# Kernel tuning notes

Measured on AMD Instinct MI355X. Metric: run time of the kernel, lower is better.

The kernel has to match this reference:

```python
import jax, jax.numpy as jnp
import numpy as np

DIM = 256
NUM_HEADS = 8
HEAD_DIM = 64
NUM_MEM_KV = 4
HIDDEN = NUM_HEADS * HEAD_DIM  # 512


def rmsnorm(x, g):
    # F.normalize(x, dim=1) * g * sqrt(C)
    c = x.shape[1]
    n = jnp.sqrt(jnp.sum(x * x, axis=1, keepdims=True))
    xn = x / jnp.maximum(n, 1e-12)
    return xn * g * (c ** 0.5)


def setup_inputs() -> dict:
    key = jax.random.key(0)
    ks = jax.random.split(key, 7)
    b, h, w = 16, 64, 64
    x = jax.random.normal(ks[0], (b, DIM, h, w), dtype=jnp.float32)
    g_in = jnp.ones((1, DIM, 1, 1), dtype=jnp.float32)
    w_qkv = jax.random.normal(ks[1], (HIDDEN * 3, DIM), dtype=jnp.float32) * (1.0 / np.sqrt(DIM))
    mem_kv = jax.random.normal(ks[2], (2, NUM_HEADS, HEAD_DIM, NUM_MEM_KV), dtype=jnp.float32)
    w_out = jax.random.normal(ks[3], (DIM, HIDDEN), dtype=jnp.float32) * (1.0 / np.sqrt(HIDDEN))
    b_out = jax.random.normal(ks[4], (DIM,), dtype=jnp.float32) * 0.01
    g_out = jnp.ones((1, DIM, 1, 1), dtype=jnp.float32)
    return {"x": x, "g_in": g_in, "w_qkv": w_qkv, "mem_kv": mem_kv,
            "w_out": w_out, "b_out": b_out, "g_out": g_out}


def reference(x, g_in, w_qkv, mem_kv, w_out, b_out, g_out):
    b, c, h, w = x.shape
    scale = HEAD_DIM ** (-0.5)
    xn = rmsnorm(x, g_in)
    # 1x1 conv (no bias) as GEMM: [b, 3*hidden, h, w]
    qkv = jnp.einsum('bcxy,oc->boxy', xn, w_qkv)
    q, k, v = jnp.split(qkv, 3, axis=1)
    # b (heads d) x y -> b heads d n
    def to_heads(t):
        return t.reshape(b, NUM_HEADS, HEAD_DIM, h * w)
    q, k, v = to_heads(q), to_heads(k), to_heads(v)
    mem_k = jnp.broadcast_to(mem_kv[0], (b, NUM_HEADS, HEAD_DIM, NUM_MEM_KV))
    mem_v = jnp.broadcast_to(mem_kv[1], (b, NUM_HEADS, HEAD_DIM, NUM_MEM_KV))
    k = jnp.concatenate([mem_k, k], axis=-1)
    v = jnp.concatenate([mem_v, v], axis=-1)
    q = jax.nn.softmax(q, axis=-2) * scale   # softmax over head_dim
    k = jax.nn.softmax(k, axis=-1)           # softmax over sequence
    context = jnp.einsum('bhdn,bhen->bhde', k, v)  # [b,h,d,d] per-head context
    out = jnp.einsum('bhde,bhdn->bhen', context, q)  # [b,h,d,n]
    out = out.reshape(b, HIDDEN, h, w)
    out = jnp.einsum('bcxy,oc->boxy', out, w_out) + b_out[None, :, None, None]
    return rmsnorm(out, g_out)
```

## Files before the change

kernel.cpp:

```cpp
#include <hip/hip_runtime.h>
#include <hip/hip_bf16.h>

typedef __hip_bfloat16 bf16;
typedef short bf16x8 __attribute__((ext_vector_type(8)));
typedef float f32x4 __attribute__((ext_vector_type(4)));

#define PTOT  65536
#define NPOS  4096
#define CIN   256
#define HID   512
#define HD    64

__device__ __forceinline__ float us2f(unsigned short u) {
    return __uint_as_float(((unsigned int)u) << 16);
}
__device__ __forceinline__ float ldf(const void* p, size_t i, bool bf) {
    return bf ? us2f(((const unsigned short*)p)[i]) : ((const float*)p)[i];
}
__device__ __forceinline__ unsigned short f2bs(float v) {
    __hip_bfloat16 h = __float2bfloat16(v);
    return *reinterpret_cast<unsigned short*>(&h);
}
__device__ __forceinline__ void gld16(const void* g, void* s) {
    __builtin_amdgcn_global_load_lds(
        (const __attribute__((address_space(1))) unsigned int*)g,
        (__attribute__((address_space(3))) unsigned int*)s, 16, 0, 0);
}

__global__ __launch_bounds__(256) void k_detect(const unsigned* __restrict__ x,
                                                int* __restrict__ flag) {
    int t = threadIdx.x;
    unsigned w = x[(size_t)t * 997];
    unsigned e7 = (w >> 8) & 0x7f;
    __shared__ int s[256];
    s[t] = (e7 >= 58 && e7 <= 66) ? 1 : 0;
    __syncthreads();
    for (int k = 128; k > 0; k >>= 1) { if (t < k) s[t] += s[t + k]; __syncthreads(); }
    if (t == 0) flag[0] = (s[0] >= 128) ? 1 : 0;
}

__global__ void k_relay(const int* __restrict__ src, int* __restrict__ dst) {
    dst[0] = src[0];
}

__global__ __launch_bounds__(256) void k_cvt(const void* __restrict__ src,
        unsigned short* __restrict__ dst, int n, const int* __restrict__ flag) {
    bool bf = flag[0] != 0;
    int i = blockIdx.x * 256 + threadIdx.x;
    if (i < n) dst[i] = f2bs(ldf(src, i, bf));
}

template<bool BF>
__device__ __forceinline__ void norm_xn_body(const void* __restrict__ x,
        const void* __restrict__ g, unsigned short* __restrict__ xn,
        float* __restrict__ smem)
{
    float* xs   = smem;
    float* gS   = smem + 17216;
    float* red2 = smem + 17472;
    float* sS   = smem + 18496;
    const int t = threadIdx.x;
    const int p0 = blockIdx.x * 64;
    const int b = p0 >> 12;
    const int posbase = p0 & 4095;
    gS[t] = ldf(g, t, BF);
    __syncthreads();
    const int pl4 = (t & 15) * 4;
    const int crow = t >> 4;
    const size_t xbase = ((size_t)b * CIN) << 12;
    float ssq[4] = {0.f, 0.f, 0.f, 0.f};
    #pragma unroll
    for (int rr = 0; rr < 16; ++rr) {
        int c = rr * 16 + crow;
        float v[4];
        if (BF) {
            ushort4 u = *(const ushort4*)((const unsigned short*)x + xbase +
                                          ((size_t)c << 12) + posbase + pl4);
            v[0] = us2f(u.x); v[1] = us2f(u.y); v[2] = us2f(u.z); v[3] = us2f(u.w);
        } else {
            float4 f = *(const float4*)((const float*)x + xbase +
                                        ((size_t)c << 12) + posbase + pl4);
            v[0] = f.x; v[1] = f.y; v[2] = f.z; v[3] = f.w;
        }
        float gv = gS[c];
        float* row = xs + (c >> 6) * 4304 + (c & 63) * 67;
        #pragma unroll
        for (int e = 0; e < 4; ++e) {
            ssq[e] += v[e] * v[e];
            row[pl4 + e] = v[e] * gv;
        }
    }
    #pragma unroll
    for (int e = 0; e < 4; ++e) red2[crow * 64 + pl4 + e] = ssq[e];
    __syncthreads();
    if (t < 64) {
        float tot = 0.f;
        #pragma unroll
        for (int j = 0; j < 16; ++j) tot += red2[j * 64 + t];
        sS[t] = 16.0f / fmaxf(sqrtf(tot), 1e-12f);
    }
    __syncthreads();
    const int pr = t >> 2, c0 = (t & 3) * 64;
    const float sc = sS[pr];
    const float* base = xs + (t & 3) * 4304 + pr;
    unsigned short* dst = &xn[(size_t)(p0 + pr) * 256 + c0];
    #pragma unroll
    for (int q = 0; q < 4; ++q) {
        unsigned short tmp[16];
        #pragma unroll
        for (int j = 0; j < 16; ++j)
            tmp[j] = f2bs(base[(q * 16 + j) * 67] * sc);
        *(uint4*)(dst + q * 16)     = ((uint4*)tmp)[0];
        *(uint4*)(dst + q * 16 + 8) = ((uint4*)tmp)[1];
    }
}
__global__ __launch_bounds__(256) void k_norm_xn(
        const void* __restrict__ x, const void* __restrict__ g,
        unsigned short* __restrict__ xn, const int* __restrict__ flag)
{
    __shared__ float smem[18560];
    if (flag[0]) norm_xn_body<true>(x, g, xn, smem);
    else         norm_xn_body<false>(x, g, xn, smem);
}

template<int KTOT, bool BIAS, int OSTRIDE>
__global__ __launch_bounds__(256) void k_mfma(
        const bf16* __restrict__ Am, const bf16* __restrict__ Bm,
        const void* __restrict__ bias, bf16* __restrict__ C,
        const int* __restrict__ flag)
{
    __shared__ __align__(16) unsigned short As[128 * 32];
    __shared__ __align__(16) unsigned short Bs[128 * 32];
    const int tid = threadIdx.x;
    const int wv = tid >> 6, lane = tid & 63;
    const int quad = lane >> 4, l16 = lane & 15;
    const int wm = wv >> 1, wn = wv & 1;
    const int m0 = blockIdx.y * 128, n0 = blockIdx.x * 128;
    f32x4 acc[4][4] = {};
    const bf16* gA = Am + (size_t)(m0 + (tid >> 2)) * KTOT + (tid & 3) * 8;
    const bf16* gB = Bm + (size_t)(n0 + (tid >> 2)) * KTOT + (tid & 3) * 8;
    unsigned short* lA = As + wv * 512;
    unsigned short* lB = Bs + wv * 512;
    for (int k0 = 0; k0 < KTOT; k0 += 32) {
        gld16(gA + k0, lA);
        gld16(gA + (size_t)64 * KTOT + k0, lA + 2048);
        gld16(gB + k0, lB);
        gld16(gB + (size_t)64 * KTOT + k0, lB + 2048);
        __syncthreads();
        bf16x8 bfr[4];
        #pragma unroll
        for (int j = 0; j < 4; ++j)
            bfr[j] = *(const bf16x8*)&Bs[(wn * 64 + j * 16 + l16) * 32 + quad * 8];
        #pragma unroll
        for (int i = 0; i < 4; ++i) {
            bf16x8 af = *(const bf16x8*)&As[(wm * 64 + i * 16 + l16) * 32 + quad * 8];
            #pragma unroll
            for (int j = 0; j < 4; ++j)
                acc[i][j] = __builtin_amdgcn_mfma_f32_16x16x32_bf16(af, bfr[j], acc[i][j], 0, 0, 0);
        }
        __syncthreads();
    }
    bool bf = BIAS ? (flag[0] != 0) : false;
    #pragma unroll
    for (int i = 0; i < 4; ++i) {
        int row = m0 + wm * 64 + i * 16 + quad * 4;
        #pragma unroll
        for (int r = 0; r < 4; ++r) {
            float bv = BIAS ? ldf(bias, row + r, bf) : 0.0f;
            #pragma unroll
            for (int j = 0; j < 4; ++j) {
                int col = n0 + wn * 64 + j * 16 + l16;
                C[(size_t)(row + r) * OSTRIDE + col] = __float2bfloat16(acc[i][j][r] + bv);
            }
        }
    }
}

__global__ __launch_bounds__(512) void k_kvgemm(
        const bf16* __restrict__ Am, const bf16* __restrict__ Bm,
        bf16* __restrict__ C)
{
    __shared__ __align__(16) unsigned short As[128 * 256];
    __shared__ __align__(16) unsigned short Bs[2][64 * 256];
    const int t = threadIdx.x;
    const int w = t >> 6, lane = t & 63;
    const int quad = lane >> 4, l16 = lane & 15;
    const int wm = w >> 1, wn = w & 1;
    const int p = blockIdx.x;
    const int xcd = p & 7, slot = p >> 3;
    const int chunk = xcd * 4 + (slot & 3);
    const int mt = slot >> 2;
    const int m0 = mt * 128;
    const size_t cbase = (size_t)chunk * 2048;

    const int srow = t >> 5;
    const int sks  = (t & 31) ^ (srow & 7);

    #pragma unroll
    for (int q = 0; q < 8; ++q)
        gld16(Am + (size_t)(m0 + q * 16 + srow) * 256 + sks * 8,
              (char*)As + q * 8192 + w * 1024);
    #pragma unroll
    for (int q = 0; q < 4; ++q)
        gld16(Bm + (cbase + q * 16 + srow) * 256 + sks * 8,
              (char*)Bs[0] + q * 8192 + w * 1024);
    #pragma unroll
    for (int q = 0; q < 4; ++q)
        gld16(Bm + (cbase + 64 + q * 16 + srow) * 256 + sks * 8,
              (char*)Bs[1] + q * 8192 + w * 1024);

    asm volatile("s_waitcnt vmcnt(8)" ::: "memory");
    __builtin_amdgcn_s_barrier();
    asm volatile("" ::: "memory");

    bf16x8 af[2][8];
    #pragma unroll
    for (int i = 0; i < 2; ++i) {
        int row = wm * 32 + i * 16 + l16;
        #pragma unroll
        for (int kk = 0; kk < 8; ++kk)
            af[i][kk] = *(const bf16x8*)((const char*)As + row * 512 +
                         (((kk * 4 + quad) ^ (row & 7)) << 4));
    }

    for (int s = 0; s < 32; ++s) {
        if (s > 0) {
            asm volatile("" ::: "memory");
            __builtin_amdgcn_s_barrier();
            asm volatile("" ::: "memory");
            if (s + 1 < 32) {
                #pragma unroll
                for (int q = 0; q < 4; ++q)
                    gld16(Bm + (cbase + (size_t)(s + 1) * 64 + q * 16 + srow) * 256 + sks * 8,
                          (char*)Bs[(s + 1) & 1] + q * 8192 + w * 1024);
            }
        }
        if (s == 0)      asm volatile("s_waitcnt vmcnt(4)"  ::: "memory");
        else if (s < 31) asm volatile("s_waitcnt vmcnt(20)" ::: "memory");
        else             asm volatile("s_waitcnt vmcnt(16)" ::: "memory");
        __builtin_amdgcn_s_barrier();
        asm volatile("" ::: "memory");

        const unsigned short* Bbuf = Bs[s & 1];
        f32x4 acc[2][2] = {};
        #pragma unroll
        for (int kk = 0; kk < 8; ++kk) {
            bf16x8 bfr[2];
            #pragma unroll
            for (int j = 0; j < 2; ++j) {
                int row = wn * 32 + j * 16 + l16;
                bfr[j] = *(const bf16x8*)((const char*)Bbuf + row * 512 +
                          (((kk * 4 + quad) ^ (row & 7)) << 4));
            }
            #pragma unroll
            for (int i = 0; i < 2; ++i)
                #pragma unroll
                for (int j = 0; j < 2; ++j)
                    acc[i][j] = __builtin_amdgcn_mfma_f32_16x16x32_bf16(af[i][kk], bfr[j], acc[i][j], 0, 0, 0);
        }
        #pragma unroll
        for (int i = 0; i < 2; ++i) {
            #pragma unroll
            for (int r = 0; r < 4; ++r) {
                int row = m0 + wm * 32 + i * 16 + quad * 4 + r;
                size_t col = cbase + (size_t)s * 64 + wn * 32;
                #pragma unroll
                for (int j = 0; j < 2; ++j)
                    C[(size_t)row * PTOT + col + j * 16 + l16] = __float2bfloat16(acc[i][j][r]);
            }
        }
    }
}

__global__ __launch_bounds__(256) void k_qapply(
        const bf16* __restrict__ xn, const bf16* __restrict__ wq,
        const unsigned short* __restrict__ ct_bf,
        unsigned short* __restrict__ oat_pe)
{
    __shared__ __align__(16) unsigned short smem[128 * 136 + 2 * 64 * 72];
    unsigned short* As  = smem;
    unsigned short* Bs  = smem + 8192;
    unsigned short* As2 = smem;
    unsigned short* ctS = smem + 17408;
    const int tid = threadIdx.x;
    const int wv = tid >> 6, lane = tid & 63;
    const int quad = lane >> 4, l16 = lane & 15;
    const int wm = wv >> 1, wn = wv & 1;
    const int n0 = blockIdx.x * 128;
    const int m0 = blockIdx.y * 128;
    const int b = m0 >> 12;

    {
        int hh = tid >> 7, tt = tid & 127;
        int bh = (b << 3) + (n0 >> 6) + hh;
        int e = tt >> 1, d0 = (tt & 1) * 32;
        const unsigned short* src = ct_bf + (size_t)bh * 4096 + e * 64 + d0;
        unsigned short* dst = ctS + hh * 4608 + e * 72 + d0;
        *(uint4*)dst        = *(const uint4*)src;
        *(uint4*)(dst + 8)  = *(const uint4*)(src + 8);
        *(uint4*)(dst + 16) = *(const uint4*)(src + 16);
        *(uint4*)(dst + 24) = *(const uint4*)(src + 24);
    }

    f32x4 acc[4][4] = {};
    const bf16* gA = xn + (size_t)(m0 + (tid >> 2)) * CIN + (tid & 3) * 8;
    const bf16* gB = wq + (size_t)(n0 + (tid >> 2)) * CIN + (tid & 3) * 8;
    unsigned short* lA = As + wv * 512;
    unsigned short* lB = Bs + wv * 512;
    for (int k0 = 0; k0 < CIN; k0 += 32) {
        gld16(gA + k0, lA);
        gld16(gA + (size_t)64 * CIN + k0, lA + 2048);
        gld16(gB + k0, lB);
        gld16(gB + (size_t)64 * CIN + k0, lB + 2048);
        __syncthreads();
        bf16x8 bfr[4];
        #pragma unroll
        for (int j = 0; j < 4; ++j)
            bfr[j] = *(const bf16x8*)&Bs[(wn * 64 + j * 16 + l16) * 32 + quad * 8];
        #pragma unroll
        for (int i = 0; i < 4; ++i) {
            bf16x8 af = *(const bf16x8*)&As[(wm * 64 + i * 16 + l16) * 32 + quad * 8];
            #pragma unroll
            for (int j = 0; j < 4; ++j)
                acc[i][j] = __builtin_amdgcn_mfma_f32_16x16x32_bf16(af, bfr[j], acc[i][j], 0, 0, 0);
        }
        __syncthreads();
    }

    #pragma unroll
    for (int i = 0; i < 4; ++i) {
        #pragma unroll
        for (int r = 0; r < 4; ++r) {
            float m = fmaxf(fmaxf(acc[i][0][r], acc[i][1][r]),
                            fmaxf(acc[i][2][r], acc[i][3][r]));
            #pragma unroll
            for (int s = 1; s < 16; s <<= 1)
                m = fmaxf(m, __shfl_xor(m, s));
            float ev[4];
            float sum = 0.f;
            #pragma unroll
            for (int j = 0; j < 4; ++j) { ev[j] = expf(acc[i][j][r] - m); sum += ev[j]; }
            #pragma unroll
            for (int s = 1; s < 16; s <<= 1)
                sum += __shfl_xor(sum, s);
            float inv = 0.125f / sum;
            int row = wm * 64 + i * 16 + quad * 4 + r;
            #pragma unroll
            for (int j = 0; j < 4; ++j)
                As2[row * 136 + wn * 64 + j * 16 + l16] = f2bs(ev[j] * inv);
        }
    }
    __syncthreads();

    f32x4 acc2[4][4] = {};
    #pragma unroll
    for (int kk = 0; kk < 2; ++kk) {
        bf16x8 bfr[4];
        #pragma unroll
        for (int j = 0; j < 4; ++j)
            bfr[j] = *(const bf16x8*)&ctS[wn * 4608 + (j * 16 + l16) * 72 + kk * 32 + quad * 8];
        #pragma unroll
        for (int i = 0; i < 4; ++i) {
            bf16x8 af = *(const bf16x8*)&As2[(wm * 64 + i * 16 + l16) * 136 + wn * 64 + kk * 32 + quad * 8];
            #pragma unroll
            for (int j = 0; j < 4; ++j)
                acc2[i][j] = __builtin_amdgcn_mfma_f32_16x16x32_bf16(af, bfr[j], acc2[i][j], 0, 0, 0);
        }
    }
    #pragma unroll
    for (int i = 0; i < 4; ++i) {
        #pragma unroll
        for (int r = 0; r < 4; ++r) {
            int prow = wm * 64 + i * 16 + quad * 4 + r;
            unsigned short* obase = oat_pe + (size_t)(m0 + prow) * HID + n0 + wn * 64;
            #pragma unroll
            for (int j = 0; j < 4; ++j)
                obase[j * 16 + l16] = f2bs(acc2[i][j][r]);
        }
    }
}

__global__ __launch_bounds__(256) void k_kstats(
        const bf16* __restrict__ kv, const void* __restrict__ memkv,
        float* __restrict__ rowmax, float* __restrict__ rowinv,
        const int* __restrict__ flag)
{
    bool bf = flag[0] != 0;
    int r = blockIdx.x;
    int b = r >> 9, hd = r & 511;
    const unsigned short* krow = (const unsigned short*)kv + (size_t)hd * PTOT + b * NPOS;
    int t = threadIdx.x;
    float vals[16];
    float m = -1e30f;
    #pragma unroll
    for (int i = 0; i < 16; ++i) {
        vals[i] = us2f(krow[t + (i << 8)]);
        m = fmaxf(m, vals[i]);
    }
    float mv = (t < 4) ? ldf(memkv, hd * 4 + t, bf) : -1e30f;
    m = fmaxf(m, mv);
    __shared__ float red[256];
    red[t] = m; __syncthreads();
    for (int s = 128; s > 0; s >>= 1) {
        if (t < s) red[t] = fmaxf(red[t], red[t + s]);
        __syncthreads();
    }
    float M = red[0]; __syncthreads();
    float sum = 0.f;
    #pragma unroll
    for (int i = 0; i < 16; ++i) sum += expf(vals[i] - M);
    if (t < 4) sum += expf(mv - M);
    red[t] = sum; __syncthreads();
    for (int s = 128; s > 0; s >>= 1) {
        if (t < s) red[t] += red[t + s];
        __syncthreads();
    }
    if (t == 0) { rowmax[r] = M; rowinv[r] = 1.0f / red[0]; }
}

__global__ __launch_bounds__(256) void k_context_mfma(
        const bf16* __restrict__ kv, const void* __restrict__ memkv,
        const float* __restrict__ rowmax, const float* __restrict__ rowinv,
        float* __restrict__ ctpart, const int* __restrict__ flag)
{
    bool bf = flag[0] != 0;
    int bh = blockIdx.x, chunk = blockIdx.y;
    int b = bh >> 3, h = bh & 7;
    __shared__ __align__(16) unsigned short As[4][64 * 32];
    __shared__ __align__(16) unsigned short Bs[4][64 * 32];
    __shared__ float rmS[64], riS[64];
    const int tid = threadIdx.x;
    if (tid < 64) {
        rmS[tid] = rowmax[(b << 9) + (h << 6) + tid];
        riS[tid] = rowinv[(b << 9) + (h << 6) + tid];
    }
    __syncthreads();
    const int wv = tid >> 6, lane = tid & 63;
    const int quad = lane >> 4, l16 = lane & 15;
    const int wm = wv >> 1, wn = wv & 1;
    const int krow = tid >> 2, kseg = tid & 3;
    const float rm = rmS[krow], ri = riS[krow];
    const unsigned short* kbase = (const unsigned short*)kv + (size_t)(h * HD) * PTOT + b * NPOS + chunk * 1024;
    const unsigned short* vbase = (const unsigned short*)kv + (size_t)(HID + h * HD) * PTOT + b * NPOS + chunk * 1024;
    f32x4 acc[2][2] = {};
    for (int s = 0; s < 8; ++s) {
        int nb = s * 128;
        #pragma unroll
        for (int kk = 0; kk < 4; ++kk) {
            uint4 u = *(const uint4*)(kbase + (size_t)krow * PTOT + nb + kk * 32 + kseg * 8);
            unsigned short out[8];
            const unsigned short* us = (const unsigned short*)&u;
            #pragma unroll
            for (int e = 0; e < 8; ++e)
                out[e] = f2bs(expf(us2f(us[e]) - rm) * ri);
            *(uint4*)&As[kk][krow * 32 + kseg * 8] = *(uint4*)out;
        }
        #pragma unroll
        for (int kk = 0; kk < 4; ++kk)
            gld16(vbase + (size_t)(wv * 16 + (lane >> 2)) * PTOT + nb + kk * 32 + (lane & 3) * 8,
                  &Bs[kk][wv * 512]);
        __syncthreads();
        #pragma unroll
        for (int kk = 0; kk < 4; ++kk) {
            bf16x8 bfr[2];
            #pragma unroll
            for (int j = 0; j < 2; ++j)
                bfr[j] = *(const bf16x8*)&Bs[kk][(wn * 32 + j * 16 + l16) * 32 + quad * 8];
            #pragma unroll
            for (int i = 0; i < 2; ++i) {
                bf16x8 af = *(const bf16x8*)&As[kk][(wm * 32 + i * 16 + l16) * 32 + quad * 8];
                #pragma unroll
                for (int j = 0; j < 2; ++j)
                    acc[i][j] = __builtin_amdgcn_mfma_f32_16x16x32_bf16(af, bfr[j], acc[i][j], 0, 0, 0);
            }
        }
        __syncthreads();
    }
    if (chunk == 0) {
        float mv[2][4];
        #pragma unroll
        for (int j = 0; j < 2; ++j) {
            int e = wn * 32 + j * 16 + l16;
            #pragma unroll
            for (int mm = 0; mm < 4; ++mm)
                mv[j][mm] = ldf(memkv, 2048 + ((h << 6) + e) * 4 + mm, bf);
        }
        #pragma unroll
        for (int i = 0; i < 2; ++i) {
            #pragma unroll
            for (int r = 0; r < 4; ++r) {
                int d = wm * 32 + i * 16 + quad * 4 + r;
                #pragma unroll
                for (int mm = 0; mm < 4; ++mm) {
                    float kw = expf(ldf(memkv, ((h << 6) + d) * 4 + mm, bf) - rmS[d]) * riS[d];
                    #pragma unroll
                    for (int j = 0; j < 2; ++j)
                        acc[i][j][r] = fmaf(kw, mv[j][mm], acc[i][j][r]);
                }
            }
        }
    }
    float* outp = ctpart + (size_t)(chunk * 128 + bh) * 4096;
    #pragma unroll
    for (int i = 0; i < 2; ++i) {
        #pragma unroll
        for (int r = 0; r < 4; ++r) {
            int d = wm * 32 + i * 16 + quad * 4 + r;
            #pragma unroll
            for (int j = 0; j < 2; ++j) {
                int e = wn * 32 + j * 16 + l16;
                outp[d * 64 + e] = acc[i][j][r];
            }
        }
    }
}

__global__ __launch_bounds__(256) void k_ctsum(
        const float* __restrict__ ctpart, unsigned short* __restrict__ ct_bf)
{
    int bh = blockIdx.x, t = threadIdx.x;
    int i0 = t * 16;
    int e = i0 >> 6, d0 = i0 & 63;
    unsigned short tmp[16];
    #pragma unroll
    for (int j = 0; j < 16; ++j) {
        int d = d0 + j;
        float s = 0.f;
        #pragma unroll
        for (int c = 0; c < 4; ++c)
            s += ctpart[(size_t)(c * 128 + bh) * 4096 + d * 64 + e];
        tmp[j] = f2bs(s);
    }
    unsigned short* dst = ct_bf + (size_t)bh * 4096 + i0;
    *(uint4*)dst = ((uint4*)tmp)[0];
    *(uint4*)(dst + 8) = ((uint4*)tmp)[1];
}

template<bool BF>
__device__ __forceinline__ void rmsout_body(const unsigned short* __restrict__ pre,
        const void* __restrict__ g, void* __restrict__ out, float* __restrict__ smem)
{
    float* gS   = smem;
    float* red2 = smem + 256;
    float* sS   = smem + 1280;
    const int t = threadIdx.x;
    const int p0 = blockIdx.x * 64;
    const int b = p0 >> 12;
    const int posbase = p0 & 4095;
    gS[t] = ldf(g, t, BF);
    const int pl4 = (t & 15) * 4;
    const int crow = t >> 4;
    const unsigned short* pbase = pre + p0 + pl4;
    ushort4 u[16];
    float ssq[4] = {0.f, 0.f, 0.f, 0.f};
    #pragma unroll
    for (int rr = 0; rr < 16; ++rr) {
        int c = rr * 16 + crow;
        u[rr] = *(const ushort4*)(pbase + (size_t)c * PTOT);
        float v0 = us2f(u[rr].x), v1 = us2f(u[rr].y), v2 = us2f(u[rr].z), v3 = us2f(u[rr].w);
        ssq[0] += v0 * v0; ssq[1] += v1 * v1; ssq[2] += v2 * v2; ssq[3] += v3 * v3;
    }
    #pragma unroll
    for (int e = 0; e < 4; ++e) red2[crow * 64 + pl4 + e] = ssq[e];
    __syncthreads();
    if (t < 64) {
        float tot = 0.f;
        #pragma unroll
        for (int j = 0; j < 16; ++j) tot += red2[j * 64 + t];
        sS[t] = 16.0f / fmaxf(sqrtf(tot), 1e-12f);
    }
    __syncthreads();
    const float s0 = sS[pl4], s1 = sS[pl4 + 1], s2 = sS[pl4 + 2], s3 = sS[pl4 + 3];
    #pragma unroll
    for (int rr = 0; rr < 16; ++rr) {
        int c = rr * 16 + crow;
        float gv = gS[c];
        float v0 = us2f(u[rr].x) * s0 * gv;
        float v1 = us2f(u[rr].y) * s1 * gv;
        float v2 = us2f(u[rr].z) * s2 * gv;
        float v3 = us2f(u[rr].w) * s3 * gv;
        size_t oi = ((size_t)(b * CIN + c) << 12) + posbase + pl4;
        if (BF) {
            ushort4 o;
            o.x = f2bs(v0); o.y = f2bs(v1); o.z = f2bs(v2); o.w = f2bs(v3);
            *(ushort4*)((unsigned short*)out + oi) = o;
        } else {
            float4 o; o.x = v0; o.y = v1; o.z = v2; o.w = v3;
            *(float4*)((float*)out + oi) = o;
        }
    }
}
__global__ __launch_bounds__(256) void k_rmsnorm_out(
        const unsigned short* __restrict__ pre, const void* __restrict__ g,
        void* __restrict__ out, const int* __restrict__ flag)
{
    __shared__ float smem[1344];
    if (flag[0]) rmsout_body<true>(pre, g, out, smem);
    else         rmsout_body<false>(pre, g, out, smem);
}

extern "C" void kernel_launch(void* const* d_in, const int* in_sizes, int n_in,
                              void* d_out, int out_size, void* d_ws, size_t ws_size,
                              hipStream_t stream) {
    const void* x     = d_in[0];
    const void* g_in  = d_in[1];
    const void* w_qkv = d_in[2];
    const void* memkv = d_in[3];
    const void* w_out = d_in[4];
    const void* b_out = d_in[5];
    const void* g_out = d_in[6];

    char* ws = (char*)d_ws;
    bf16*           kv     = (bf16*)ws;
    unsigned short* oat_pe = (unsigned short*)(ws + 67108864);
    unsigned short* pre    = (unsigned short*)ws;
    int*            flagB  = (int*)(ws + 50331648);

    char* ob = (char*)d_out;
    float*          ctpart = (float*)ob;
    float*          rowmax = (float*)(ob + 8388608);
    float*          rowinv = (float*)(ob + 8421376);
    int*            flagA  = (int*)(ob + 8454144);
    unsigned short* wq_b   = (unsigned short*)(ob + 9437184);
    unsigned short* wout_b = (unsigned short*)(ob + 10485760);
    unsigned short* ct_bf  = (unsigned short*)(ob + 11010048);
    unsigned short* xn     = (unsigned short*)(ob + 12582912);

    k_detect<<<1, 256, 0, stream>>>((const unsigned*)x, flagA);

    k_cvt<<<1536, 256, 0, stream>>>(w_qkv, wq_b, 1536 * 256, flagA);
    k_cvt<<<512, 256, 0, stream>>>(w_out, wout_b, 256 * 512, flagA);

    k_norm_xn<<<1024, 256, 0, stream>>>(x, g_in, xn, flagA);

    k_kvgemm<<<256, 512, 0, stream>>>(
        (const bf16*)(wq_b + (size_t)512 * CIN), (const bf16*)xn, kv);

    k_kstats<<<8192, 256, 0, stream>>>(kv, memkv, rowmax, rowinv, flagA);

    dim3 gctx(128, 4);
    k_context_mfma<<<gctx, 256, 0, stream>>>(kv, memkv, rowmax, rowinv, ctpart, flagA);

    k_ctsum<<<128, 256, 0, stream>>>(ctpart, ct_bf);

    dim3 gqa(4, 512);
    k_qapply<<<gqa, 256, 0, stream>>>(
        (const bf16*)xn, (const bf16*)wq_b, ct_bf, oat_pe);

    dim3 go(512, 2);
    k_mfma<HID, true, PTOT><<<go, 256, 0, stream>>>(
        (const bf16*)wout_b, (const bf16*)oat_pe, b_out, (bf16*)pre, flagA);

    k_relay<<<1, 1, 0, stream>>>(flagA, flagB);

    k_rmsnorm_out<<<1024, 256, 0, stream>>>(pre, g_out, d_out, flagB);
}
```

Measured before the change: 351.3 us.

## Restructure q-apply kernel as persistent weight-resident loop with double-buffered xn tiles

The q-projection, softmax and context-apply kernel now launches 256 blocks of 512 threads. Each block keeps its 128-channel weight slice and two heads' context matrices resident in 144KB of LDS, loaded once through XOR-swizzled direct-to-LDS loads. It then streams 16 tiles of 64 positions, double-buffering the xn loads with explicit vmcnt waits. The softmax goes through an fp32 staging buffer in LDS. This avoids reloading weights and context for every 128-position tile, at the cost of much lower occupancy, extra barriers per tile and smaller MFMA tiles per wave.

```diff
diff --git a/kernel.cpp b/kernel.cpp
--- a/kernel.cpp
+++ b/kernel.cpp
@@ -272,110 +272,174 @@
     }
 }
 
-__global__ __launch_bounds__(256) void k_qapply(
+__global__ __launch_bounds__(512) void k_qapply(
         const bf16* __restrict__ xn, const bf16* __restrict__ wq,
         const unsigned short* __restrict__ ct_bf,
         unsigned short* __restrict__ oat_pe)
 {
-    __shared__ __align__(16) unsigned short smem[128 * 136 + 2 * 64 * 72];
-    unsigned short* As  = smem;
-    unsigned short* Bs  = smem + 8192;
-    unsigned short* As2 = smem;
-    unsigned short* ctS = smem + 17408;
-    const int tid = threadIdx.x;
-    const int wv = tid >> 6, lane = tid & 63;
+    __shared__ __align__(16) char smem[147456];
+    unsigned short* As  = (unsigned short*)smem;
+    unsigned short* Bs  = (unsigned short*)(smem + 65536);
+    unsigned short* ctS = (unsigned short*)(smem + 131072);
+    float*          S32 = (float*)smem;
+    unsigned short* qsm = (unsigned short*)(smem + 33792);
+    const int t = threadIdx.x;
+    const int w = t >> 6, lane = t & 63;
     const int quad = lane >> 4, l16 = lane & 15;
-    const int wm = wv >> 1, wn = wv & 1;
-    const int n0 = blockIdx.x * 128;
-    const int m0 = blockIdx.y * 128;
-    const int b = m0 >> 12;
-
-    {
-        int hh = tid >> 7, tt = tid & 127;
-        int bh = (b << 3) + (n0 >> 6) + hh;
-        int e = tt >> 1, d0 = (tt & 1) * 32;
-        const unsigned short* src = ct_bf + (size_t)bh * 4096 + e * 64 + d0;
-        unsigned short* dst = ctS + hh * 4608 + e * 72 + d0;
-        *(uint4*)dst        = *(const uint4*)src;
-        *(uint4*)(dst + 8)  = *(const uint4*)(src + 8);
-        *(uint4*)(dst + 16) = *(const uint4*)(src + 16);
-        *(uint4*)(dst + 24) = *(const uint4*)(src + 24);
-    }
-
-    f32x4 acc[4][4] = {};
-    const bf16* gA = xn + (size_t)(m0 + (tid >> 2)) * CIN + (tid & 3) * 8;
-    const bf16* gB = wq + (size_t)(n0 + (tid >> 2)) * CIN + (tid & 3) * 8;
-    unsigned short* lA = As + wv * 512;
-    unsigned short* lB = Bs + wv * 512;
-    for (int k0 = 0; k0 < CIN; k0 += 32) {
-        gld16(gA + k0, lA);
-        gld16(gA + (size_t)64 * CIN + k0, lA + 2048);
-        gld16(gB + k0, lB);
-        gld16(gB + (size_t)64 * CIN + k0, lB + 2048);
-        __syncthreads();
-        bf16x8 bfr[4];
-        #pragma unroll
-        for (int j = 0; j < 4; ++j)
-            bfr[j] = *(const bf16x8*)&Bs[(wn * 64 + j * 16 + l16) * 32 + quad * 8];
-        #pragma unroll
-        for (int i = 0; i < 4; ++i) {
-            bf16x8 af = *(const bf16x8*)&As[(wm * 64 + i * 16 + l16) * 32 + quad * 8];
-            #pragma unroll
-            for (int j = 0; j < 4; ++j)
-                acc[i][j] = __builtin_amdgcn_mfma_f32_16x16x32_bf16(af, bfr[j], acc[i][j], 0, 0, 0);
-        }
-        __syncthreads();
-    }
-
-    #pragma unroll
-    for (int i = 0; i < 4; ++i) {
-        #pragma unroll
-        for (int r = 0; r < 4; ++r) {
-            float m = fmaxf(fmaxf(acc[i][0][r], acc[i][1][r]),
-                            fmaxf(acc[i][2][r], acc[i][3][r]));
-            #pragma unroll
-            for (int s = 1; s < 16; s <<= 1)
-                m = fmaxf(m, __shfl_xor(m, s));
-            float ev[4];
-            float sum = 0.f;
-            #pragma unroll
-            for (int j = 0; j < 4; ++j) { ev[j] = expf(acc[i][j][r] - m); sum += ev[j]; }
-            #pragma unroll
-            for (int s = 1; s < 16; s <<= 1)
-                sum += __shfl_xor(sum, s);
+    const int wm = w >> 1, wn = w & 1;
+    const int ct4 = blockIdx.x & 3;
+    const int chunk = blockIdx.x >> 2;
+    const int n0 = ct4 * 128;
+    const size_t P0 = (size_t)chunk * 1024;
+    const int b = (int)(P0 >> 12);
+    const int srow = t >> 5, sks = (t & 31) ^ (srow & 7);
+
+    #pragma unroll
+    for (int q = 0; q < 8; ++q)
+        gld16(wq + (size_t)(n0 + q * 16 + srow) * 256 + sks * 8,
+              smem + q * 8192 + w * 1024);
+    #pragma unroll
+    for (int k = 0; k < 2; ++k) {
+        int u = k * 512 + t;
+        int hh = u >> 9, e = (u >> 3) & 63, slot = u & 7;
+        gld16(ct_bf + (size_t)(b * 8 + ct4 * 2 + hh) * 4096 + e * 64 + ((slot ^ (e & 7)) * 8),
+              (char*)ctS + k * 8192 + w * 1024);
+    }
+    #pragma unroll
+    for (int q = 0; q < 4; ++q)
+        gld16(xn + (P0 + q * 16 + srow) * 256 + sks * 8,
+              (char*)Bs + q * 8192 + w * 1024);
+    #pragma unroll
+    for (int q = 0; q < 4; ++q)
+        gld16(xn + (P0 + 64 + q * 16 + srow) * 256 + sks * 8,
+              (char*)Bs + 32768 + q * 8192 + w * 1024);
+
+    asm volatile("s_waitcnt vmcnt(10)" ::: "memory");
+    __builtin_amdgcn_s_barrier();
+    asm volatile("" ::: "memory");
+
+    bf16x8 af[2][8];
+    #pragma unroll
+    for (int i = 0; i < 2; ++i) {
+        int row = wm * 32 + i * 16 + l16;
+        #pragma unroll
+        for (int kk = 0; kk < 8; ++kk)
+            af[i][kk] = *(const bf16x8*)((const char*)As + row * 512 +
+                         (((kk * 4 + quad) ^ (row & 7)) << 4));
+    }
+
+    const int smrow = t >> 2, smseg = t & 3;
+    const int smpos = smrow >> 1, smhead = smrow & 1;
+    const int hh = w >> 2, pm = (w >> 1) & 1, pn = w & 1;
+
+    for (int s = 0; s < 16; ++s) {
+        if (s > 0 && s + 1 < 16) {
+            #pragma unroll
+            for (int q = 0; q < 4; ++q)
+                gld16(xn + (P0 + (size_t)(s + 1) * 64 + q * 16 + srow) * 256 + sks * 8,
+                      (char*)Bs + ((s + 1) & 1) * 32768 + q * 8192 + w * 1024);
+        }
+        if (s == 0)      asm volatile("s_waitcnt vmcnt(4)"  ::: "memory");
+        else if (s < 15) asm volatile("s_waitcnt vmcnt(20)" ::: "memory");
+        else             asm volatile("s_waitcnt vmcnt(16)" ::: "memory");
+        __builtin_amdgcn_s_barrier();
+        asm volatile("" ::: "memory");
+
+        const char* Bbuf = (const char*)Bs + (s & 1) * 32768;
+        f32x4 acc[2][2] = {};
+        #pragma unroll
+        for (int kk = 0; kk < 8; ++kk) {
+            bf16x8 bfr[2];
+            #pragma unroll
+            for (int j = 0; j < 2; ++j) {
+                int row = wn * 32 + j * 16 + l16;
+                bfr[j] = *(const bf16x8*)(Bbuf + row * 512 +
+                          (((kk * 4 + quad) ^ (row & 7)) << 4));
+            }
+            #pragma unroll
+            for (int i = 0; i < 2; ++i)
+                #pragma unroll
+                for (int j = 0; j < 2; ++j)
+                    acc[i][j] = __builtin_amdgcn_mfma_f32_16x16x32_bf16(af[i][kk], bfr[j], acc[i][j], 0, 0, 0);
+        }
+        #pragma unroll
+        for (int i = 0; i < 2; ++i)
+            #pragma unroll
+            for (int j = 0; j < 2; ++j) {
+                int pos = wn * 32 + j * 16 + l16;
+                int chb = wm * 32 + i * 16 + quad * 4;
+                #pragma unroll
+                for (int r = 0; r < 4; ++r)
+                    S32[pos * 132 + chb + r] = acc[i][j][r];
+            }
+        asm volatile("s_waitcnt lgkmcnt(0)" ::: "memory");
+        __builtin_amdgcn_s_barrier();
+        asm volatile("" ::: "memory");
+
+        {
+            const float* srp = S32 + smpos * 132 + smhead * 64 + smseg * 16;
+            f32x4 v[4];
+            #pragma unroll
+            for (int q = 0; q < 4; ++q) v[q] = *(const f32x4*)(srp + q * 4);
+            float m = v[0][0];
+            #pragma unroll
+            for (int q = 0; q < 4; ++q)
+                #pragma unroll
+                for (int e = 0; e < 4; ++e) m = fmaxf(m, v[q][e]);
+            m = fmaxf(m, __shfl_xor(m, 1));
+            m = fmaxf(m, __shfl_xor(m, 2));
+            float ev[16], sum = 0.f;
+            #pragma unroll
+            for (int q = 0; q < 4; ++q)
+                #pragma unroll
+                for (int e = 0; e < 4; ++e) {
+                    float x = expf(v[q][e] - m);
+                    ev[q * 4 + e] = x; sum += x;
+                }
+            sum += __shfl_xor(sum, 1);
+            sum += __shfl_xor(sum, 2);
             float inv = 0.125f / sum;
-            int row = wm * 64 + i * 16 + quad * 4 + r;
-            #pragma unroll
-            for (int j = 0; j < 4; ++j)
-                As2[row * 136 + wn * 64 + j * 16 + l16] = f2bs(ev[j] * inv);
-        }
-    }
-    __syncthreads();
-
-    f32x4 acc2[4][4] = {};
-    #pragma unroll
-    for (int kk = 0; kk < 2; ++kk) {
-        bf16x8 bfr[4];
-        #pragma unroll
-        for (int j = 0; j < 4; ++j)
-            bfr[j] = *(const bf16x8*)&ctS[wn * 4608 + (j * 16 + l16) * 72 + kk * 32 + quad * 8];
-        #pragma unroll
-        for (int i = 0; i < 4; ++i) {
-            bf16x8 af = *(const bf16x8*)&As2[(wm * 64 + i * 16 + l16) * 136 + wn * 64 + kk * 32 + quad * 8];
-            #pragma unroll
-            for (int j = 0; j < 4; ++j)
-                acc2[i][j] = __builtin_amdgcn_mfma_f32_16x16x32_bf16(af, bfr[j], acc2[i][j], 0, 0, 0);
-        }
-    }
-    #pragma unroll
-    for (int i = 0; i < 4; ++i) {
-        #pragma unroll
-        for (int r = 0; r < 4; ++r) {
-            int prow = wm * 64 + i * 16 + quad * 4 + r;
-            unsigned short* obase = oat_pe + (size_t)(m0 + prow) * HID + n0 + wn * 64;
-            #pragma unroll
-            for (int j = 0; j < 4; ++j)
-                obase[j * 16 + l16] = f2bs(acc2[i][j][r]);
+            unsigned short tmp[16];
+            #pragma unroll
+            for (int q = 0; q < 16; ++q) tmp[q] = f2bs(ev[q] * inv);
+            unsigned short* dq = qsm + smpos * 136 + smhead * 64 + smseg * 16;
+            *(uint4*)dq       = ((uint4*)tmp)[0];
+            *(uint4*)(dq + 8) = ((uint4*)tmp)[1];
+        }
+        asm volatile("s_waitcnt lgkmcnt(0)" ::: "memory");
+        __builtin_amdgcn_s_barrier();
+        asm volatile("" ::: "memory");
+
+        f32x4 acc2[2][2] = {};
+        #pragma unroll
+        for (int kk = 0; kk < 2; ++kk) {
+            bf16x8 a2[2], b2[2];
+            #pragma unroll
+            for (int i = 0; i < 2; ++i)
+                a2[i] = *(const bf16x8*)&qsm[(pm * 32 + i * 16 + l16) * 136 +
+                                             hh * 64 + kk * 32 + quad * 8];
+            #pragma unroll
+            for (int j = 0; j < 2; ++j) {
+                int e = pn * 32 + j * 16 + l16;
+                b2[j] = *(const bf16x8*)&ctS[hh * 4096 + e * 64 +
+                         (((kk * 4 + quad) ^ (e & 7)) * 8)];
+            }
+            #pragma unroll
+            for (int i = 0; i < 2; ++i)
+                #pragma unroll
+                for (int j = 0; j < 2; ++j)
+                    acc2[i][j] = __builtin_amdgcn_mfma_f32_16x16x32_bf16(a2[i], b2[j], acc2[i][j], 0, 0, 0);
+        }
+        #pragma unroll
+        for (int i = 0; i < 2; ++i) {
+            #pragma unroll
+            for (int r = 0; r < 4; ++r) {
+                size_t prow = P0 + (size_t)s * 64 + pm * 32 + i * 16 + quad * 4 + r;
+                unsigned short* obase = oat_pe + prow * HID + n0 + hh * 64 + pn * 32;
+                #pragma unroll
+                for (int j = 0; j < 2; ++j)
+                    obase[j * 16 + l16] = f2bs(acc2[i][j][r]);
+            }
         }
     }
 }
@@ -643,8 +707,7 @@
 
     k_ctsum<<<128, 256, 0, stream>>>(ctpart, ct_bf);
 
-    dim3 gqa(4, 512);
-    k_qapply<<<gqa, 256, 0, stream>>>(
+    k_qapply<<<256, 512, 0, stream>>>(
         (const bf16*)xn, (const bf16*)wq_b, ct_bf, oat_pe);
 
     dim3 go(512, 2);
```

New measurement: 350.0 us. Within noise of the previous version (-0.4%).

## Restructure q-apply kernel into per-head persistent blocks with double-buffered xn tiles

Applied to the files above, without the earlier changes.

The q-projection/softmax/context-apply kernel is rewritten so each 512-thread block owns one head and a 1024-position chunk. The head's 64x256 weight slice is held in registers and the context matrix in swizzled LDS, while xn tiles stream through a double-buffered LDS pipeline with explicit waitcnt and barrier control. This removes the repeated weight and context reloads and LDS bank conflicts of the old 128x128 tiling, at the cost of three barriers per 32-position step and smaller MFMA work per step. Separately, expf is replaced by the fast __expf intrinsic in the kstats and context kernels.

```diff
diff --git a/kernel.cpp b/kernel.cpp
--- a/kernel.cpp
+++ b/kernel.cpp
@@ -272,110 +272,132 @@
     }
 }
 
-__global__ __launch_bounds__(256) void k_qapply(
+__global__ __launch_bounds__(512, 4) void k_qapply(
         const bf16* __restrict__ xn, const bf16* __restrict__ wq,
         const unsigned short* __restrict__ ct_bf,
         unsigned short* __restrict__ oat_pe)
 {
-    __shared__ __align__(16) unsigned short smem[128 * 136 + 2 * 64 * 72];
-    unsigned short* As  = smem;
-    unsigned short* Bs  = smem + 8192;
-    unsigned short* As2 = smem;
-    unsigned short* ctS = smem + 17408;
-    const int tid = threadIdx.x;
-    const int wv = tid >> 6, lane = tid & 63;
+    __shared__ __align__(16) char smem[73728];
+    unsigned short* As  = (unsigned short*)smem;
+    float*          S32 = (float*)smem;
+    unsigned short* qsm = (unsigned short*)(smem + 8192);
+    unsigned short* Bs  = (unsigned short*)(smem + 32768);
+    unsigned short* ctS = (unsigned short*)(smem + 65536);
+    const int t = threadIdx.x;
+    const int w = t >> 6, lane = t & 63;
     const int quad = lane >> 4, l16 = lane & 15;
-    const int wm = wv >> 1, wn = wv & 1;
-    const int n0 = blockIdx.x * 128;
-    const int m0 = blockIdx.y * 128;
-    const int b = m0 >> 12;
-
+    const int wm = w >> 1, wn = w & 1;
+    const int pm = w >> 2, pn = w & 3;
+    const int bid = blockIdx.x;
+    const int h = (bid >> 3) & 7;
+    const int c = (bid & 7) | ((bid >> 6) << 3);
+    const int n0 = h * HD;
+    const size_t P0 = (size_t)c * 1024;
+    const int b = (int)(P0 >> 12);
+    const int srow = t >> 5, sks = (t & 31) ^ (srow & 7);
+
+    #pragma unroll
+    for (int q = 0; q < 4; ++q)
+        gld16(wq + (size_t)(n0 + q * 16 + srow) * 256 + sks * 8,
+              smem + q * 8192 + w * 1024);
     {
-        int hh = tid >> 7, tt = tid & 127;
-        int bh = (b << 3) + (n0 >> 6) + hh;
-        int e = tt >> 1, d0 = (tt & 1) * 32;
-        const unsigned short* src = ct_bf + (size_t)bh * 4096 + e * 64 + d0;
-        unsigned short* dst = ctS + hh * 4608 + e * 72 + d0;
-        *(uint4*)dst        = *(const uint4*)src;
-        *(uint4*)(dst + 8)  = *(const uint4*)(src + 8);
-        *(uint4*)(dst + 16) = *(const uint4*)(src + 16);
-        *(uint4*)(dst + 24) = *(const uint4*)(src + 24);
-    }
-
-    f32x4 acc[4][4] = {};
-    const bf16* gA = xn + (size_t)(m0 + (tid >> 2)) * CIN + (tid & 3) * 8;
-    const bf16* gB = wq + (size_t)(n0 + (tid >> 2)) * CIN + (tid & 3) * 8;
-    unsigned short* lA = As + wv * 512;
-    unsigned short* lB = Bs + wv * 512;
-    for (int k0 = 0; k0 < CIN; k0 += 32) {
-        gld16(gA + k0, lA);
-        gld16(gA + (size_t)64 * CIN + k0, lA + 2048);
-        gld16(gB + k0, lB);
-        gld16(gB + (size_t)64 * CIN + k0, lB + 2048);
-        __syncthreads();
-        bf16x8 bfr[4];
-        #pragma unroll
-        for (int j = 0; j < 4; ++j)
-            bfr[j] = *(const bf16x8*)&Bs[(wn * 64 + j * 16 + l16) * 32 + quad * 8];
-        #pragma unroll
-        for (int i = 0; i < 4; ++i) {
-            bf16x8 af = *(const bf16x8*)&As[(wm * 64 + i * 16 + l16) * 32 + quad * 8];
-            #pragma unroll
-            for (int j = 0; j < 4; ++j)
-                acc[i][j] = __builtin_amdgcn_mfma_f32_16x16x32_bf16(af, bfr[j], acc[i][j], 0, 0, 0);
-        }
-        __syncthreads();
-    }
-
-    #pragma unroll
-    for (int i = 0; i < 4; ++i) {
+        int e = t >> 3, sl = t & 7;
+        gld16(ct_bf + (size_t)(b * 8 + h) * 4096 + e * 64 + ((sl ^ (e & 7)) * 8),
+              (char*)ctS + w * 1024);
+    }
+    #pragma unroll
+    for (int q = 0; q < 2; ++q)
+        gld16(xn + (P0 + q * 16 + srow) * 256 + sks * 8,
+              (char*)Bs + q * 8192 + w * 1024);
+    #pragma unroll
+    for (int q = 0; q < 2; ++q)
+        gld16(xn + (P0 + 32 + q * 16 + srow) * 256 + sks * 8,
+              (char*)Bs + 16384 + q * 8192 + w * 1024);
+
+    asm volatile("s_waitcnt vmcnt(4)" ::: "memory");
+    __builtin_amdgcn_s_barrier();
+    asm volatile("" ::: "memory");
+
+    bf16x8 af[8];
+    {
+        int row = wm * 16 + l16;
+        #pragma unroll
+        for (int kk = 0; kk < 8; ++kk)
+            af[kk] = *(const bf16x8*)((const char*)As + row * 512 +
+                      (((kk * 4 + quad) ^ (row & 7)) << 4));
+    }
+
+    const int smp = t >> 4, smseg = t & 15;
+
+    for (int s = 0; s < 32; ++s) {
+        if (s > 0 && s + 1 < 32) {
+            #pragma unroll
+            for (int q = 0; q < 2; ++q)
+                gld16(xn + (P0 + (size_t)(s + 1) * 32 + q * 16 + srow) * 256 + sks * 8,
+                      (char*)Bs + ((s + 1) & 1) * 16384 + q * 8192 + w * 1024);
+        }
+        if (s == 0)      asm volatile("s_waitcnt vmcnt(2)" ::: "memory");
+        else if (s < 31) asm volatile("s_waitcnt vmcnt(6)" ::: "memory");
+        else             asm volatile("s_waitcnt vmcnt(4)" ::: "memory");
+        __builtin_amdgcn_s_barrier();
+        asm volatile("" ::: "memory");
+
+        const char* Bbuf = (const char*)Bs + (s & 1) * 16384;
+        f32x4 acc = {};
+        #pragma unroll
+        for (int kk = 0; kk < 8; ++kk) {
+            int row = wn * 16 + l16;
+            bf16x8 bfr = *(const bf16x8*)(Bbuf + row * 512 +
+                          (((kk * 4 + quad) ^ (row & 7)) << 4));
+            acc = __builtin_amdgcn_mfma_f32_16x16x32_bf16(af[kk], bfr, acc, 0, 0, 0);
+        }
+        {
+            int pos = wn * 16 + l16;
+            int sl = (wm * 4 + quad) ^ (pos & 7);
+            *(f32x4*)&S32[pos * 64 + sl * 4] = acc;
+        }
+        asm volatile("s_waitcnt lgkmcnt(0)" ::: "memory");
+        __builtin_amdgcn_s_barrier();
+        asm volatile("" ::: "memory");
+
+        {
+            f32x4 v = *(const f32x4*)&S32[smp * 64 + ((smseg ^ (smp & 7)) << 2)];
+            float m = fmaxf(fmaxf(v[0], v[1]), fmaxf(v[2], v[3]));
+            #pragma unroll
+            for (int st = 1; st < 16; st <<= 1)
+                m = fmaxf(m, __shfl_xor(m, st));
+            float ev[4], sum = 0.f;
+            #pragma unroll
+            for (int e = 0; e < 4; ++e) { ev[e] = __expf(v[e] - m); sum += ev[e]; }
+            #pragma unroll
+            for (int st = 1; st < 16; st <<= 1)
+                sum += __shfl_xor(sum, st);
+            float inv = 0.125f / sum;
+            unsigned short tmp[4];
+            #pragma unroll
+            for (int e = 0; e < 4; ++e) tmp[e] = f2bs(ev[e] * inv);
+            *(ushort4*)&qsm[smp * 64 + (((smseg >> 1) ^ (smp & 7)) << 3) + (smseg & 1) * 4]
+                = *(ushort4*)tmp;
+        }
+        asm volatile("s_waitcnt lgkmcnt(0)" ::: "memory");
+        __builtin_amdgcn_s_barrier();
+        asm volatile("" ::: "memory");
+
+        f32x4 acc2 = {};
+        #pragma unroll
+        for (int kk = 0; kk < 2; ++kk) {
+            int prow = pm * 16 + l16;
+            bf16x8 a2 = *(const bf16x8*)&qsm[prow * 64 +
+                         (((kk * 4 + quad) ^ (prow & 7)) << 3)];
+            int e = pn * 16 + l16;
+            bf16x8 b2 = *(const bf16x8*)&ctS[e * 64 +
+                         (((kk * 4 + quad) ^ (e & 7)) << 3)];
+            acc2 = __builtin_amdgcn_mfma_f32_16x16x32_bf16(a2, b2, acc2, 0, 0, 0);
+        }
         #pragma unroll
         for (int r = 0; r < 4; ++r) {
-            float m = fmaxf(fmaxf(acc[i][0][r], acc[i][1][r]),
-                            fmaxf(acc[i][2][r], acc[i][3][r]));
-            #pragma unroll
-            for (int s = 1; s < 16; s <<= 1)
-                m = fmaxf(m, __shfl_xor(m, s));
-            float ev[4];
-            float sum = 0.f;
-            #pragma unroll
-            for (int j = 0; j < 4; ++j) { ev[j] = expf(acc[i][j][r] - m); sum += ev[j]; }
-            #pragma unroll
-            for (int s = 1; s < 16; s <<= 1)
-                sum += __shfl_xor(sum, s);
-            float inv = 0.125f / sum;
-            int row = wm * 64 + i * 16 + quad * 4 + r;
-            #pragma unroll
-            for (int j = 0; j < 4; ++j)
-                As2[row * 136 + wn * 64 + j * 16 + l16] = f2bs(ev[j] * inv);
-        }
-    }
-    __syncthreads();
-
-    f32x4 acc2[4][4] = {};
-    #pragma unroll
-    for (int kk = 0; kk < 2; ++kk) {
-        bf16x8 bfr[4];
-        #pragma unroll
-        for (int j = 0; j < 4; ++j)
-            bfr[j] = *(const bf16x8*)&ctS[wn * 4608 + (j * 16 + l16) * 72 + kk * 32 + quad * 8];
-        #pragma unroll
-        for (int i = 0; i < 4; ++i) {
-            bf16x8 af = *(const bf16x8*)&As2[(wm * 64 + i * 16 + l16) * 136 + wn * 64 + kk * 32 + quad * 8];
-            #pragma unroll
-            for (int j = 0; j < 4; ++j)
-                acc2[i][j] = __builtin_amdgcn_mfma_f32_16x16x32_bf16(af, bfr[j], acc2[i][j], 0, 0, 0);
-        }
-    }
-    #pragma unroll
-    for (int i = 0; i < 4; ++i) {
-        #pragma unroll
-        for (int r = 0; r < 4; ++r) {
-            int prow = wm * 64 + i * 16 + quad * 4 + r;
-            unsigned short* obase = oat_pe + (size_t)(m0 + prow) * HID + n0 + wn * 64;
-            #pragma unroll
-            for (int j = 0; j < 4; ++j)
-                obase[j * 16 + l16] = f2bs(acc2[i][j][r]);
+            size_t prow = P0 + (size_t)s * 32 + pm * 16 + quad * 4 + r;
+            oat_pe[prow * HID + n0 + pn * 16 + l16] = f2bs(acc2[r]);
         }
     }
 }
@@ -408,8 +430,8 @@
     float M = red[0]; __syncthreads();
     float sum = 0.f;
     #pragma unroll
-    for (int i = 0; i < 16; ++i) sum += expf(vals[i] - M);
-    if (t < 4) sum += expf(mv - M);
+    for (int i = 0; i < 16; ++i) sum += __expf(vals[i] - M);
+    if (t < 4) sum += __expf(mv - M);
     red[t] = sum; __syncthreads();
     for (int s = 128; s > 0; s >>= 1) {
         if (t < s) red[t] += red[t + s];
@@ -452,7 +474,7 @@
             const unsigned short* us = (const unsigned short*)&u;
             #pragma unroll
             for (int e = 0; e < 8; ++e)
-                out[e] = f2bs(expf(us2f(us[e]) - rm) * ri);
+                out[e] = f2bs(__expf(us2f(us[e]) - rm) * ri);
             *(uint4*)&As[kk][krow * 32 + kseg * 8] = *(uint4*)out;
         }
         #pragma unroll
@@ -492,7 +514,7 @@
                 int d = wm * 32 + i * 16 + quad * 4 + r;
                 #pragma unroll
                 for (int mm = 0; mm < 4; ++mm) {
-                    float kw = expf(ldf(memkv, ((h << 6) + d) * 4 + mm, bf) - rmS[d]) * riS[d];
+                    float kw = __expf(ldf(memkv, ((h << 6) + d) * 4 + mm, bf) - rmS[d]) * riS[d];
                     #pragma unroll
                     for (int j = 0; j < 2; ++j)
                         acc[i][j][r] = fmaf(kw, mv[j][mm], acc[i][j][r]);
@@ -643,8 +665,7 @@
 
     k_ctsum<<<128, 256, 0, stream>>>(ctpart, ct_bf);
 
-    dim3 gqa(4, 512);
-    k_qapply<<<gqa, 256, 0, stream>>>(
+    k_qapply<<<512, 512, 0, stream>>>(
         (const bf16*)xn, (const bf16*)wq_b, ct_bf, oat_pe);
 
     dim3 go(512, 2);
```

After: 336.7 us. 4.2% less time.
